# Kernel tuning notes

Hardware: AMD Instinct MI355X
Metric: run time of the kernel (lower is better)

The kernel has to match this reference:

```python
import jax, jax.numpy as jnp
import numpy as np

H = 4          # hidden_size
NUM_LAYERS = 5
SEQ = 610
BATCH = 128


def _lstm_layer(x, w_i, w_h, bi, bh):
    # x: [B, T, I]; w_i: [4H, I]; w_h: [4H, H]; bi, bh: [4H]
    # PyTorch gate order: i, f, g, o
    B = x.shape[0]
    b = bi + bh

    def step(carry, xt):
        h, c = carry
        gates = xt @ w_i.T + h @ w_h.T + b          # [B, 4H]
        i, f, g, o = jnp.split(gates, 4, axis=-1)
        c = jax.nn.sigmoid(f) * c + jax.nn.sigmoid(i) * jnp.tanh(g)
        h = jax.nn.sigmoid(o) * jnp.tanh(c)
        return (h, c), h

    h0 = jnp.zeros((B, H), x.dtype)
    c0 = jnp.zeros((B, H), x.dtype)
    (_, _), hs = jax.lax.scan(step, (h0, c0), jnp.swapaxes(x, 0, 1))  # hs: [T, B, H]
    return jnp.swapaxes(hs, 0, 1)                   # [B, T, H]


def setup_inputs() -> dict:
    key = jax.random.key(0)
    ks = jax.random.split(key, 10)
    s = 1.0 / np.sqrt(H)  # PyTorch default uniform(-1/sqrt(H), 1/sqrt(H))
    u = lambda k, shape: jax.random.uniform(k, shape, jnp.float32, -s, s)
    return {
        "x": jax.random.normal(ks[0], (BATCH, SEQ, 2), jnp.float32),
        "w_ih0": u(ks[1], (4 * H, 2)),
        "w_ih": u(ks[2], (NUM_LAYERS - 1, 4 * H, H)),
        "w_hh": u(ks[3], (NUM_LAYERS, 4 * H, H)),
        "b_ih": u(ks[4], (NUM_LAYERS, 4 * H)),
        "b_hh": u(ks[5], (NUM_LAYERS, 4 * H)),
        "w_lin": u(ks[6], (1, H)),
        "b_lin": u(ks[7], (1,)),
        "w_fc": jax.random.uniform(ks[8], (5, SEQ), jnp.float32, -1.0 / np.sqrt(SEQ), 1.0 / np.sqrt(SEQ)),
        "b_fc": jax.random.uniform(ks[9], (5,), jnp.float32, -1.0 / np.sqrt(SEQ), 1.0 / np.sqrt(SEQ)),
    }


def reference(x, w_ih0, w_ih, w_hh, b_ih, b_hh, w_lin, b_lin, w_fc, b_fc):
    # 5-layer stacked LSTM, zero initial state (as on the module's first call)
    out = _lstm_layer(x, w_ih0, w_hh[0], b_ih[0], b_hh[0])
    for l in range(NUM_LAYERS - 1):
        out = _lstm_layer(out, w_ih[l], w_hh[l + 1], b_ih[l + 1], b_hh[l + 1])
    # per-timestep Linear(4 -> 1) then cat along dim 1 -> [B, T]
    t = (out @ w_lin.T + b_lin)[..., 0]             # [B, 610]
    return t @ w_fc.T + b_fc                         # [B, 5]
```

## Files before the change

### kernel.cpp

```cpp
#include <hip/hip_runtime.h>
#include <math.h>

#define H 4
#define NL 5
#define SEQ 610
#define BATCH 128
#define NITER 619
#define HEAD 10

template<int CTRL, bool BC>
__device__ __forceinline__ float dpp1(float old_, float src) {
    return __int_as_float(__builtin_amdgcn_update_dpp(
        __float_as_int(old_), __float_as_int(src), CTRL, 0xF, 0xF, BC));
}

__global__ __launch_bounds__(64) void lstm_sp_kernel(
    const float* __restrict__ x,
    const float* __restrict__ w_ih0,
    const float* __restrict__ w_ih,
    const float* __restrict__ w_hh,
    const float* __restrict__ b_ih,
    const float* __restrict__ b_hh,
    const float* __restrict__ w_lin,
    const float* __restrict__ b_lin,
    const float* __restrict__ w_fc,
    const float* __restrict__ b_fc,
    float* __restrict__ out)
{
    __shared__ float lds_x[2 * SEQ * 2 + 24];
    __shared__ float lds_wfcp[4 * SEQ * 2];

    const int lane = threadIdx.x;
    const int half = lane >> 5;
    const int r    = lane & 31;
    const int l    = r >> 2;
    const int k    = r & 3;
    const int lw   = l > 4 ? 4 : l;
    const bool is_l0 = (l == 0);
    const int row  = blockIdx.x * 2 + half;

    #pragma unroll
    for (int hh = 0; hh < 2; ++hh) {
        const float4* src = (const float4*)(x + (size_t)(blockIdx.x * 2 + hh) * (SEQ * 2));
        float4* dst = (float4*)&lds_x[hh * (SEQ * 2)];
        for (int i = lane; i < (SEQ * 2) / 4; i += 64) dst[i] = src[i];
    }
    #pragma unroll
    for (int kk = 0; kk < 4; ++kk) {
        for (int t = lane; t < SEQ; t += 64) {
            lds_wfcp[(kk * SEQ + t) * 2 + 0] = w_fc[kk * SEQ + t];
            lds_wfcp[(kk * SEQ + t) * 2 + 1] = w_fc[4 * SEQ + t];
        }
    }
    __syncthreads();

    float wi[4][4], wh[4][4], bias[4];
    #pragma unroll
    for (int j = 0; j < 4; ++j) {
        const float s = (j == 2) ? 2.8853900817779268f
                                 : -1.4426950408889634f;
        const int wrow = j * H + k;
        if (lw == 0) {
            wi[j][0] = w_ih0[wrow * 2 + 0] * s;
            wi[j][1] = w_ih0[wrow * 2 + 1] * s;
            wi[j][2] = 0.f; wi[j][3] = 0.f;
        } else {
            const float4 v = *(const float4*)&w_ih[((lw - 1) * 16 + wrow) * 4];
            wi[j][0] = v.x * s; wi[j][1] = v.y * s; wi[j][2] = v.z * s; wi[j][3] = v.w * s;
        }
        const float4 u = *(const float4*)&w_hh[(lw * 16 + wrow) * 4];
        wh[j][0] = u.x * s; wh[j][1] = u.y * s; wh[j][2] = u.z * s; wh[j][3] = u.w * s;
        bias[j] = (b_ih[lw * 16 + wrow] + b_hh[lw * 16 + wrow]) * s;
    }
    const float wl0 = w_lin[0], wl1 = w_lin[1], wl2 = w_lin[2], wl3 = w_lin[3];
    const float bl  = b_lin[0];

    const int xb     = half * (SEQ * 2);
    const int wpbase = k * SEQ;

    float c = 0.f;
    float q0 = 0.f, q1 = 0.f, q2 = 0.f, q3 = 0.f;
    float accA = 0.f, accB = 0.f;
    float pre0, pre1, pre2, pre3;
    {
        const float2 xv0 = *(const float2*)&lds_x[xb];
        const float xq0 = is_l0 ? xv0.x : 0.f;
        const float xq1 = is_l0 ? xv0.y : 0.f;
        pre0 = fmaf(wi[0][1], xq1, fmaf(wi[0][0], xq0, bias[0]));
        pre1 = fmaf(wi[1][1], xq1, fmaf(wi[1][0], xq0, bias[1]));
        pre2 = fmaf(wi[2][1], xq1, fmaf(wi[2][0], xq0, bias[2]));
        pre3 = fmaf(wi[3][1], xq1, fmaf(wi[3][0], xq0, bias[3]));
    }

    #define TICK_BODY(tau_, GATED)                                                    \
    {                                                                                 \
                                   \
        const float2 nx = *(const float2*)&lds_x[xb + ((tau_) + 1) * 2];              \
        int t4 = (tau_) - 9;                                                          \
        if (GATED) t4 = t4 < 0 ? 0 : t4;                                              \
        const float2 wv = *(const float2*)&lds_wfcp[(wpbase + t4) * 2];               \
                                              \
        const float oq0 = q0, oq1 = q1, oq2 = q2, oq3 = q3;                           \
                  \
        const float g0 = fmaf(wh[0][3], oq3, fmaf(wh[0][2], oq2, fmaf(wh[0][1], oq1, fmaf(wh[0][0], oq0, pre0)))); \
        const float g1 = fmaf(wh[1][3], oq3, fmaf(wh[1][2], oq2, fmaf(wh[1][1], oq1, fmaf(wh[1][0], oq0, pre1)))); \
        const float g2 = fmaf(wh[2][3], oq3, fmaf(wh[2][2], oq2, fmaf(wh[2][1], oq1, fmaf(wh[2][0], oq0, pre2)))); \
        const float g3 = fmaf(wh[3][3], oq3, fmaf(wh[3][2], oq2, fmaf(wh[3][1], oq1, fmaf(wh[3][0], oq0, pre3)))); \
        const float Ai = 1.f + __builtin_amdgcn_exp2f(g0);                            \
        const float Af = 1.f + __builtin_amdgcn_exp2f(g1);                            \
        const float Dg = 1.f + __builtin_amdgcn_exp2f(g2);                            \
        const float Ao = 1.f + __builtin_amdgcn_exp2f(g3);                            \
        const float M   = Ai * Dg;                                                    \
        const float den = M * Af;                                                     \
        const float num = fmaf(c, M, Af * (Dg - 2.f));                                \
        float cn = num * __builtin_amdgcn_rcpf(den);                                  \
        if (GATED) { const unsigned tt = (unsigned)((tau_) - 2 * l);                  \
                     cn = (tt < SEQ) ? cn : 0.f; }                                    \
        c = cn;                                                                       \
        const float Dc = 1.f + __builtin_amdgcn_exp2f(c * 2.8853900817779268f);       \
        const float h  = (Dc - 2.f) * __builtin_amdgcn_rcpf(Ao * Dc);                 \
        q0 = dpp1<0x00, true>(0.f, h);                                                \
        q1 = dpp1<0x55, true>(0.f, h);                                                \
        q2 = dpp1<0xAA, true>(0.f, h);                                                \
        q3 = dpp1<0xFF, true>(0.f, h);                                                \
                \
        float p0 = dpp1<0x142, true>(0.f, oq0); p0 = dpp1<0x114, false>(p0, oq0);     \
        float p1 = dpp1<0x142, true>(0.f, oq1); p1 = dpp1<0x114, false>(p1, oq1);     \
        float p2 = dpp1<0x142, true>(0.f, oq2); p2 = dpp1<0x114, false>(p2, oq2);     \
        float p3 = dpp1<0x142, true>(0.f, oq3); p3 = dpp1<0x114, false>(p3, oq3);     \
        const float xq0 = is_l0 ? nx.x : p0;                                          \
        const float xq1 = is_l0 ? nx.y : p1;                                          \
        pre0 = fmaf(wi[0][3], p3, fmaf(wi[0][2], p2, fmaf(wi[0][1], xq1, fmaf(wi[0][0], xq0, bias[0])))); \
        pre1 = fmaf(wi[1][3], p3, fmaf(wi[1][2], p2, fmaf(wi[1][1], xq1, fmaf(wi[1][0], xq0, bias[1])))); \
        pre2 = fmaf(wi[2][3], p3, fmaf(wi[2][2], p2, fmaf(wi[2][1], xq1, fmaf(wi[2][0], xq0, bias[2])))); \
        pre3 = fmaf(wi[3][3], p3, fmaf(wi[3][2], p2, fmaf(wi[3][1], xq1, fmaf(wi[3][0], xq0, bias[3])))); \
        float tval = fmaf(oq0, wl0, fmaf(oq1, wl1, fmaf(oq2, wl2, fmaf(oq3, wl3, bl)))); \
        if (GATED) tval = ((unsigned)((tau_) - 9) < SEQ) ? tval : 0.f;                \
        accA = fmaf(tval, wv.x, accA);                                                \
        accB = fmaf(tval, wv.y, accB);                                                \
    }

    for (int tau = 0; tau < HEAD; ++tau) TICK_BODY(tau, true);
    #pragma unroll 2
    for (int tau = HEAD; tau < NITER; ++tau) TICK_BODY(tau, false);
    #undef TICK_BODY

    if (r >= 16 && r < 20) {
        out[row * 5 + k] = accA + b_fc[k];
        if (k == 0) out[row * 5 + 4] = accB + b_fc[4];
    }
}

extern "C" void kernel_launch(void* const* d_in, const int* in_sizes, int n_in,
                              void* d_out, int out_size, void* d_ws, size_t ws_size,
                              hipStream_t stream)
{
    const float* x     = (const float*)d_in[0];
    const float* w_ih0 = (const float*)d_in[1];
    const float* w_ih  = (const float*)d_in[2];
    const float* w_hh  = (const float*)d_in[3];
    const float* b_ih  = (const float*)d_in[4];
    const float* b_hh  = (const float*)d_in[5];
    const float* w_lin = (const float*)d_in[6];
    const float* b_lin = (const float*)d_in[7];
    const float* w_fc  = (const float*)d_in[8];
    const float* b_fc  = (const float*)d_in[9];
    float* out = (float*)d_out;

    lstm_sp_kernel<<<dim3(BATCH / 2), dim3(64), 0, stream>>>(
        x, w_ih0, w_ih, w_hh, b_ih, b_hh, w_lin, b_lin, w_fc, b_fc, out);
}
```

Before: 176.6 us.

## Pack gate FMAs into v2f pairs and batch LDS loads per 8-step chunk

Gate pre-activations and recurrent matvecs are computed as paired 2-wide FMAs so the compiler can emit packed FP32 FMA instructions, roughly halving the FMA count on the serial critical path. The main time loop is restructured into 8-step chunks whose x and w_fc LDS loads are issued together up front, taking load latency off each step. A gated tail loop handles the final steps. This raises register pressure and code size.

After: 158.9 us. 1.11x faster.

```diff
diff --git a/kernel.cpp b/kernel.cpp
--- a/kernel.cpp
+++ b/kernel.cpp
@@ -6,7 +6,20 @@
 #define SEQ 610
 #define BATCH 128
 #define NITER 619
-#define HEAD 10
+#define HEAD 16
+#define TAIL0 616
+
+typedef float v2f __attribute__((ext_vector_type(2)));
+
+#if __has_builtin(__builtin_elementwise_fma)
+#define FMA2(a, b, c) __builtin_elementwise_fma((a), (b), (c))
+#else
+static __device__ __forceinline__ v2f FMA2(v2f a, v2f b, v2f c) {
+    v2f r; r[0] = fmaf(a[0], b[0], c[0]); r[1] = fmaf(a[1], b[1], c[1]); return r;
+}
+#endif
+
+static __device__ __forceinline__ v2f splat2(float a) { v2f r; r[0] = a; r[1] = a; return r; }
 
 template<int CTRL, bool BC>
 __device__ __forceinline__ float dpp1(float old_, float src) {
@@ -14,7 +27,7 @@
         __float_as_int(old_), __float_as_int(src), CTRL, 0xF, 0xF, BC));
 }
 
-__global__ __launch_bounds__(64) void lstm_sp_kernel(
+__global__ __launch_bounds__(64) void lstm_pk_kernel(
     const float* __restrict__ x,
     const float* __restrict__ w_ih0,
     const float* __restrict__ w_ih,
@@ -27,8 +40,8 @@
     const float* __restrict__ b_fc,
     float* __restrict__ out)
 {
-    __shared__ float lds_x[2 * SEQ * 2 + 24];
-    __shared__ float lds_wfcp[4 * SEQ * 2];
+    __shared__ float lds_x[2 * SEQ * 2 + 32];
+    __shared__ float lds_wfcp[4 * SEQ * 2 + 8];
 
     const int lane = threadIdx.x;
     const int half = lane >> 5;
@@ -54,23 +67,35 @@
     }
     __syncthreads();
 
-    float wi[4][4], wh[4][4], bias[4];
-    #pragma unroll
-    for (int j = 0; j < 4; ++j) {
-        const float s = (j == 2) ? 2.8853900817779268f
-                                 : -1.4426950408889634f;
-        const int wrow = j * H + k;
-        if (lw == 0) {
-            wi[j][0] = w_ih0[wrow * 2 + 0] * s;
-            wi[j][1] = w_ih0[wrow * 2 + 1] * s;
-            wi[j][2] = 0.f; wi[j][3] = 0.f;
-        } else {
-            const float4 v = *(const float4*)&w_ih[((lw - 1) * 16 + wrow) * 4];
-            wi[j][0] = v.x * s; wi[j][1] = v.y * s; wi[j][2] = v.z * s; wi[j][3] = v.w * s;
-        }
-        const float4 u = *(const float4*)&w_hh[(lw * 16 + wrow) * 4];
-        wh[j][0] = u.x * s; wh[j][1] = u.y * s; wh[j][2] = u.z * s; wh[j][3] = u.w * s;
-        bias[j] = (b_ih[lw * 16 + wrow] + b_hh[lw * 16 + wrow]) * s;
+    v2f wip01[4], wip23[4], whp01[4], whp23[4], b01, b23;
+    {
+        float wi[4][4], wh[4][4], bias[4];
+        #pragma unroll
+        for (int j = 0; j < 4; ++j) {
+            const float s = (j == 2) ? 2.8853900817779268f
+                                     : -1.4426950408889634f;
+            const int wrow = j * H + k;
+            if (lw == 0) {
+                wi[j][0] = w_ih0[wrow * 2 + 0] * s;
+                wi[j][1] = w_ih0[wrow * 2 + 1] * s;
+                wi[j][2] = 0.f; wi[j][3] = 0.f;
+            } else {
+                const float4 v = *(const float4*)&w_ih[((lw - 1) * 16 + wrow) * 4];
+                wi[j][0] = v.x * s; wi[j][1] = v.y * s; wi[j][2] = v.z * s; wi[j][3] = v.w * s;
+            }
+            const float4 u = *(const float4*)&w_hh[(lw * 16 + wrow) * 4];
+            wh[j][0] = u.x * s; wh[j][1] = u.y * s; wh[j][2] = u.z * s; wh[j][3] = u.w * s;
+            bias[j] = (b_ih[lw * 16 + wrow] + b_hh[lw * 16 + wrow]) * s;
+        }
+        #pragma unroll
+        for (int m = 0; m < 4; ++m) {
+            wip01[m][0] = wi[0][m]; wip01[m][1] = wi[1][m];
+            wip23[m][0] = wi[2][m]; wip23[m][1] = wi[3][m];
+            whp01[m][0] = wh[0][m]; whp01[m][1] = wh[1][m];
+            whp23[m][0] = wh[2][m]; whp23[m][1] = wh[3][m];
+        }
+        b01[0] = bias[0]; b01[1] = bias[1];
+        b23[0] = bias[2]; b23[1] = bias[3];
     }
     const float wl0 = w_lin[0], wl1 = w_lin[1], wl2 = w_lin[2], wl3 = w_lin[3];
     const float bl  = b_lin[0];
@@ -81,35 +106,27 @@
     float c = 0.f;
     float q0 = 0.f, q1 = 0.f, q2 = 0.f, q3 = 0.f;
     float accA = 0.f, accB = 0.f;
-    float pre0, pre1, pre2, pre3;
+    v2f pre01, pre23;
     {
         const float2 xv0 = *(const float2*)&lds_x[xb];
-        const float xq0 = is_l0 ? xv0.x : 0.f;
-        const float xq1 = is_l0 ? xv0.y : 0.f;
-        pre0 = fmaf(wi[0][1], xq1, fmaf(wi[0][0], xq0, bias[0]));
-        pre1 = fmaf(wi[1][1], xq1, fmaf(wi[1][0], xq0, bias[1]));
-        pre2 = fmaf(wi[2][1], xq1, fmaf(wi[2][0], xq0, bias[2]));
-        pre3 = fmaf(wi[3][1], xq1, fmaf(wi[3][0], xq0, bias[3]));
-    }
-
-    #define TICK_BODY(tau_, GATED)                                                    \
+        const float xs0 = is_l0 ? xv0.x : 0.f;
+        const float xs1 = is_l0 ? xv0.y : 0.f;
+        pre01 = FMA2(wip01[1], splat2(xs1), FMA2(wip01[0], splat2(xs0), b01));
+        pre23 = FMA2(wip23[1], splat2(xs1), FMA2(wip23[0], splat2(xs0), b23));
+    }
+
+    #define TICK_CORE(tau_, GATED, NXv, WVv)                                          \
     {                                                                                 \
-                                   \
-        const float2 nx = *(const float2*)&lds_x[xb + ((tau_) + 1) * 2];              \
-        int t4 = (tau_) - 9;                                                          \
-        if (GATED) t4 = t4 < 0 ? 0 : t4;                                              \
-        const float2 wv = *(const float2*)&lds_wfcp[(wpbase + t4) * 2];               \
-                                              \
         const float oq0 = q0, oq1 = q1, oq2 = q2, oq3 = q3;                           \
-                  \
-        const float g0 = fmaf(wh[0][3], oq3, fmaf(wh[0][2], oq2, fmaf(wh[0][1], oq1, fmaf(wh[0][0], oq0, pre0)))); \
-        const float g1 = fmaf(wh[1][3], oq3, fmaf(wh[1][2], oq2, fmaf(wh[1][1], oq1, fmaf(wh[1][0], oq0, pre1)))); \
-        const float g2 = fmaf(wh[2][3], oq3, fmaf(wh[2][2], oq2, fmaf(wh[2][1], oq1, fmaf(wh[2][0], oq0, pre2)))); \
-        const float g3 = fmaf(wh[3][3], oq3, fmaf(wh[3][2], oq2, fmaf(wh[3][1], oq1, fmaf(wh[3][0], oq0, pre3)))); \
-        const float Ai = 1.f + __builtin_amdgcn_exp2f(g0);                            \
-        const float Af = 1.f + __builtin_amdgcn_exp2f(g1);                            \
-        const float Dg = 1.f + __builtin_amdgcn_exp2f(g2);                            \
-        const float Ao = 1.f + __builtin_amdgcn_exp2f(g3);                            \
+                             \
+        v2f G01 = FMA2(whp01[3], splat2(oq3), FMA2(whp01[2], splat2(oq2),             \
+                  FMA2(whp01[1], splat2(oq1), FMA2(whp01[0], splat2(oq0), pre01)))); \
+        v2f G23 = FMA2(whp23[3], splat2(oq3), FMA2(whp23[2], splat2(oq2),             \
+                  FMA2(whp23[1], splat2(oq1), FMA2(whp23[0], splat2(oq0), pre23)))); \
+        const float Ai = 1.f + __builtin_amdgcn_exp2f(G01[0]);                        \
+        const float Af = 1.f + __builtin_amdgcn_exp2f(G01[1]);                        \
+        const float Dg = 1.f + __builtin_amdgcn_exp2f(G23[0]);                        \
+        const float Ao = 1.f + __builtin_amdgcn_exp2f(G23[1]);                        \
         const float M   = Ai * Dg;                                                    \
         const float den = M * Af;                                                     \
         const float num = fmaf(c, M, Af * (Dg - 2.f));                                \
@@ -118,32 +135,55 @@
                      cn = (tt < SEQ) ? cn : 0.f; }                                    \
         c = cn;                                                                       \
         const float Dc = 1.f + __builtin_amdgcn_exp2f(c * 2.8853900817779268f);       \
-        const float h  = (Dc - 2.f) * __builtin_amdgcn_rcpf(Ao * Dc);                 \
-        q0 = dpp1<0x00, true>(0.f, h);                                                \
-        q1 = dpp1<0x55, true>(0.f, h);                                                \
-        q2 = dpp1<0xAA, true>(0.f, h);                                                \
-        q3 = dpp1<0xFF, true>(0.f, h);                                                \
-                \
+        const float hv = (Dc - 2.f) * __builtin_amdgcn_rcpf(Ao * Dc);                 \
+        q0 = dpp1<0x00, true>(0.f, hv);                                               \
+        q1 = dpp1<0x55, true>(0.f, hv);                                               \
+        q2 = dpp1<0xAA, true>(0.f, hv);                                               \
+        q3 = dpp1<0xFF, true>(0.f, hv);                                               \
+                               \
         float p0 = dpp1<0x142, true>(0.f, oq0); p0 = dpp1<0x114, false>(p0, oq0);     \
         float p1 = dpp1<0x142, true>(0.f, oq1); p1 = dpp1<0x114, false>(p1, oq1);     \
         float p2 = dpp1<0x142, true>(0.f, oq2); p2 = dpp1<0x114, false>(p2, oq2);     \
         float p3 = dpp1<0x142, true>(0.f, oq3); p3 = dpp1<0x114, false>(p3, oq3);     \
-        const float xq0 = is_l0 ? nx.x : p0;                                          \
-        const float xq1 = is_l0 ? nx.y : p1;                                          \
-        pre0 = fmaf(wi[0][3], p3, fmaf(wi[0][2], p2, fmaf(wi[0][1], xq1, fmaf(wi[0][0], xq0, bias[0])))); \
-        pre1 = fmaf(wi[1][3], p3, fmaf(wi[1][2], p2, fmaf(wi[1][1], xq1, fmaf(wi[1][0], xq0, bias[1])))); \
-        pre2 = fmaf(wi[2][3], p3, fmaf(wi[2][2], p2, fmaf(wi[2][1], xq1, fmaf(wi[2][0], xq0, bias[2])))); \
-        pre3 = fmaf(wi[3][3], p3, fmaf(wi[3][2], p2, fmaf(wi[3][1], xq1, fmaf(wi[3][0], xq0, bias[3])))); \
+        const float xs0 = is_l0 ? (NXv).x : p0;                                       \
+        const float xs1 = is_l0 ? (NXv).y : p1;                                       \
+        pre01 = FMA2(wip01[3], splat2(p3), FMA2(wip01[2], splat2(p2),                 \
+                FMA2(wip01[1], splat2(xs1), FMA2(wip01[0], splat2(xs0), b01))));      \
+        pre23 = FMA2(wip23[3], splat2(p3), FMA2(wip23[2], splat2(p2),                 \
+                FMA2(wip23[1], splat2(xs1), FMA2(wip23[0], splat2(xs0), b23))));      \
         float tval = fmaf(oq0, wl0, fmaf(oq1, wl1, fmaf(oq2, wl2, fmaf(oq3, wl3, bl)))); \
         if (GATED) tval = ((unsigned)((tau_) - 9) < SEQ) ? tval : 0.f;                \
-        accA = fmaf(tval, wv.x, accA);                                                \
-        accB = fmaf(tval, wv.y, accB);                                                \
-    }
-
-    for (int tau = 0; tau < HEAD; ++tau) TICK_BODY(tau, true);
-    #pragma unroll 2
-    for (int tau = HEAD; tau < NITER; ++tau) TICK_BODY(tau, false);
-    #undef TICK_BODY
+        accA = fmaf(tval, (WVv).x, accA);                                             \
+        accB = fmaf(tval, (WVv).y, accB);                                             \
+    }
+
+    for (int tau = 0; tau < HEAD; ++tau) {
+        const float2 nx = *(const float2*)&lds_x[xb + (tau + 1) * 2];
+        int t4 = tau - 9; t4 = t4 < 0 ? 0 : t4;
+        const float2 wv = *(const float2*)&lds_wfcp[(wpbase + t4) * 2];
+        TICK_CORE(tau, true, nx, wv);
+    }
+
+    for (int ch = 0; ch < 75; ++ch) {
+        const int tau0 = HEAD + ch * 8;
+        float2 xc[8], wc[8];
+        #pragma unroll
+        for (int i = 0; i < 8; ++i) {
+            xc[i] = *(const float2*)&lds_x[xb + (tau0 + 1 + i) * 2];
+            wc[i] = *(const float2*)&lds_wfcp[(wpbase + tau0 + i - 9) * 2];
+        }
+        #pragma unroll
+        for (int i = 0; i < 8; ++i) {
+            TICK_CORE(tau0 + i, false, xc[i], wc[i]);
+        }
+    }
+
+    for (int tau = TAIL0; tau < NITER; ++tau) {
+        const float2 nx = *(const float2*)&lds_x[xb + (tau + 1) * 2];
+        const float2 wv = *(const float2*)&lds_wfcp[(wpbase + tau - 9) * 2];
+        TICK_CORE(tau, true, nx, wv);
+    }
+    #undef TICK_CORE
 
     if (r >= 16 && r < 20) {
         out[row * 5 + k] = accA + b_fc[k];
@@ -167,6 +207,6 @@
     const float* b_fc  = (const float*)d_in[9];
     float* out = (float*)d_out;
 
-    lstm_sp_kernel<<<dim3(BATCH / 2), dim3(64), 0, stream>>>(
+    lstm_pk_kernel<<<dim3(BATCH / 2), dim3(64), 0, stream>>>(
         x, w_ih0, w_ih, w_hh, b_ih, b_hh, w_lin, b_lin, w_fc, b_fc, out);
 }
```
